# Kernel optimization log

Hardware: AMD Instinct MI355X
Metric: run time of the kernel (lower is better)

The kernel has to match this reference:

```python
import jax, jax.numpy as jnp
import numpy as np

PATCH_SIZE = 128
NUM_PATCHES = 4


def setup_inputs() -> dict:
    key = jax.random.key(0)
    k1, k2 = jax.random.split(key)
    B, C, H, W = 32, 3, 512, 512
    images = jax.random.normal(k1, (B, C, H, W), dtype=jnp.float32)
    uncertainty_maps = jax.random.uniform(k2, (B, 1, H, W), dtype=jnp.float32)
    return {"images": images, "uncertainty_maps": uncertainty_maps}


def _select_patches(umap):
    """Greedy masked-argmax patch selection on one [H, W] uncertainty map.
    Returns coords [NUM_PATCHES, 4] int32 as (x1, y1, x2, y2)."""
    H, W = umap.shape
    eps = min(PATCH_SIZE, H // 2, W // 2)   # effective patch size (static)
    half = eps // 2
    margin = max(eps // 4, 1)
    ys = jnp.arange(H)[:, None]
    xs = jnp.arange(W)[None, :]

    def fix(a1, a2, L):
        # enforce window of exactly `eps` when clipped at the border
        small = (a2 - a1) < eps
        a2n = jnp.where(a1 == 0, jnp.minimum(L, a1 + eps), a2)
        a1n = jnp.where(a1 == 0, a1, jnp.maximum(0, a2 - eps))
        return jnp.where(small, a1n, a1), jnp.where(small, a2n, a2)

    def step(mask, _):
        masked = jnp.where(mask, -jnp.inf, umap)
        idx = jnp.argmax(masked)            # row-major first-max, same as np.ma.argmax
        yc = idx // W
        xc = idx % W
        x1 = jnp.maximum(0, xc - half)
        x2 = jnp.minimum(W, xc + half)
        y1 = jnp.maximum(0, yc - half)
        y2 = jnp.minimum(H, yc + half)
        x1, x2 = fix(x1, x2, W)
        y1, y2 = fix(y1, y2, H)
        # suppress selected region plus margin (clamping implicit in comparisons)
        box = (ys >= y1 - margin) & (ys < y2 + margin) & (xs >= x1 - margin) & (xs < x2 + margin)
        coords = jnp.stack([x1, y1, x2, y2]).astype(jnp.int32)
        return mask | box, coords

    _, coords = jax.lax.scan(step, jnp.zeros((H, W), dtype=bool), None, length=NUM_PATCHES)
    return coords  # [NUM_PATCHES, 4]


def _extract(images, coords):
    B, C, H, W = images.shape
    eps = min(PATCH_SIZE, H // 2, W // 2)

    def crop_one(img, c):
        # img [C,H,W], c = (x1,y1,x2,y2); window is always exactly eps x eps
        p = jax.lax.dynamic_slice(img, (0, c[1], c[0]), (C, eps, eps))
        if eps != PATCH_SIZE:
            # bilinear, matches F.interpolate(align_corners=False)
            p = jax.image.resize(p, (C, PATCH_SIZE, PATCH_SIZE), method="bilinear")
        return p

    return jax.vmap(jax.vmap(crop_one, in_axes=(None, 0)), in_axes=(0, 0))(images, coords)


def reference(images, uncertainty_maps):
    coords = jax.vmap(_select_patches)(uncertainty_maps[:, 0])   # [B, N, 4] int32
    patches = _extract(images, coords)                           # [B, N, C, P, P]
    return patches, coords.astype(jnp.float32)
```

## Files before the change

### kernel.cpp

```cpp
#include <hip/hip_runtime.h>
#include <math.h>
#include <float.h>

#define BN 32
#define CH 3
#define HH 512
#define WW 512
#define NP 4
#define EPS 128
#define HALF 64
#define MARGIN 32

#define NT 4096
#define PATCH_ELEMS (BN * NP * CH * EPS * EPS)
#define F4_PER_MAP (NP * CH * EPS * EPS / 4)
#define NSLICE 16
#define F4_PER_SLICE (F4_PER_MAP / NSLICE)
#define K1_NTHR 256
#define K1_NBLK (BN * NT / K1_NTHR)
#define EX_NBLK (BN * NSLICE)

__global__ __launch_bounds__(K1_NTHR)
void tile_scan(const float* __restrict__ umaps, float2* __restrict__ tiles)
{
    const int g  = blockIdx.x * K1_NTHR + threadIdx.x;
    const int b  = g >> 12;
    const int t  = g & (NT - 1);
    const int tx = t & 63, ty = t >> 6;
    const float* __restrict__ um = umaps + (size_t)b * HH * WW;
    const int x0 = tx << 3, y0 = ty << 3;
    float bv = -INFINITY; int bi = 0x7fffffff;
    #pragma unroll
    for (int r = 0; r < 8; ++r) {
        const int rowbase = (y0 + r) * WW + x0;
        const float4 a = *(const float4*)(um + rowbase);
        const float4 c = *(const float4*)(um + rowbase + 4);
        if (a.x > bv) { bv = a.x; bi = rowbase + 0; }
        if (a.y > bv) { bv = a.y; bi = rowbase + 1; }
        if (a.z > bv) { bv = a.z; bi = rowbase + 2; }
        if (a.w > bv) { bv = a.w; bi = rowbase + 3; }
        if (c.x > bv) { bv = c.x; bi = rowbase + 4; }
        if (c.y > bv) { bv = c.y; bi = rowbase + 5; }
        if (c.z > bv) { bv = c.z; bi = rowbase + 6; }
        if (c.w > bv) { bv = c.w; bi = rowbase + 7; }
    }
    tiles[g] = make_float2(bv, __int_as_float(bi));
}

__global__ __launch_bounds__(1024)
void select_k(const float* __restrict__ umaps,
              const float2* __restrict__ tiles,
              float* __restrict__ out,
              int2* __restrict__ sxy)
{
    const int tid   = threadIdx.x;
    const int lane  = tid & 63;
    const int wave  = tid >> 6;
    const int b     = blockIdx.x;
    const float* __restrict__ um = umaps + (size_t)b * HH * WW;
    float* coords_out = out + PATCH_ELEMS;

    __shared__ float2 tvi[NT];
    __shared__ int   boxes[NP][4];
    __shared__ float rv[16];
    __shared__ int   ri[16];

    {
        const float4* __restrict__ src = (const float4*)(tiles + (size_t)b * NT);
        float4* dst = (float4*)tvi;
        dst[tid]        = src[tid];
        dst[tid + 1024] = src[tid + 1024];
    }
    if (tid < NP) {
        boxes[tid][0] = 0; boxes[tid][1] = 0; boxes[tid][2] = 0; boxes[tid][3] = 0;
    }
    __syncthreads();

    for (int k = 0; k < NP; ++k) {
        float bv = -INFINITY; int bi = 0x7fffffff;
        #pragma unroll
        for (int i = 0; i < 4; ++i) {
            const float2 e = tvi[tid + (i << 10)];
            const float v = e.x; const int x = __float_as_int(e.y);
            if (v > bv || (v == bv && x < bi)) { bv = v; bi = x; }
        }
        #pragma unroll
        for (int off = 32; off > 0; off >>= 1) {
            float ov = __shfl_down(bv, off);
            int   oi = __shfl_down(bi, off);
            if (ov > bv || (ov == bv && oi < bi)) { bv = ov; bi = oi; }
        }
        if (lane == 0) { rv[wave] = bv; ri[wave] = bi; }
        __syncthreads();

        if (tid == 0) {
            bv = rv[0]; bi = ri[0];
            #pragma unroll
            for (int w = 1; w < 16; ++w)
                if (rv[w] > bv || (rv[w] == bv && ri[w] < bi)) { bv = rv[w]; bi = ri[w]; }
            const int yc = bi >> 9, xc = bi & 511;
            int x1 = max(0, xc - HALF), x2 = min(WW, xc + HALF);
            int y1 = max(0, yc - HALF), y2 = min(HH, yc + HALF);
            if (x2 - x1 < EPS) { if (x1 == 0) x2 = EPS; else x1 = x2 - EPS; }
            if (y2 - y1 < EPS) { if (y1 == 0) y2 = EPS; else y1 = y2 - EPS; }
            boxes[k][0] = max(x1 - MARGIN, 0);
            boxes[k][1] = min(x2 + MARGIN, WW);
            boxes[k][2] = max(y1 - MARGIN, 0);
            boxes[k][3] = min(y2 + MARGIN, HH);

            const int o = (b * NP + k) * 4;
            coords_out[o + 0] = (float)x1;
            coords_out[o + 1] = (float)y1;
            coords_out[o + 2] = (float)x2;
            coords_out[o + 3] = (float)y2;
            sxy[b * NP + k] = make_int2(x1, y1);
        }
        __syncthreads();

        if (k == NP - 1) break;

        const int ex1 = boxes[k][0], ex2 = boxes[k][1];
        const int ey1 = boxes[k][2], ey2 = boxes[k][3];
        const int tx1 = ex1 >> 3, tx2 = (ex2 - 1) >> 3;
        const int ty1 = ey1 >> 3, ty2 = (ey2 - 1) >> 3;
        const int wt  = tx2 - tx1 + 1;
        const int nt2 = wt * (ty2 - ty1 + 1);
        if (tid < nt2) {
            const int tx = tx1 + tid % wt;
            const int ty = ty1 + tid / wt;
            const int t  = (ty << 6) + tx;
            const int X1 = tx << 3, Y1 = ty << 3;
            if (X1 >= ex1 && X1 + 8 <= ex2 && Y1 >= ey1 && Y1 + 8 <= ey2) {
                tvi[t] = make_float2(-INFINITY, __int_as_float(0x7fffffff));
            } else {
                unsigned xm[NP]; int byl[NP], byh[NP];
                #pragma unroll
                for (int j = 0; j < NP; ++j) {
                    const int lo = min(max(boxes[j][0] - X1, 0), 8);
                    const int hi = min(max(boxes[j][1] - X1, 0), 8);
                    xm[j]  = (0xFFu << lo) & (0xFFu >> (8 - hi));
                    byl[j] = boxes[j][2]; byh[j] = boxes[j][3];
                }
                float nv = -INFINITY; int ni = 0x7fffffff;
                #pragma unroll
                for (int r = 0; r < 8; ++r) {
                    const int y = Y1 + r;
                    unsigned m8 = 0;
                    #pragma unroll
                    for (int j = 0; j < NP; ++j)
                        m8 |= (y >= byl[j] && y < byh[j]) ? xm[j] : 0u;
                    const int rowbase = y * WW + X1;
                    const float4 a = *(const float4*)(um + rowbase);
                    const float4 c = *(const float4*)(um + rowbase + 4);
                    const float vals[8] = {a.x, a.y, a.z, a.w, c.x, c.y, c.z, c.w};
                    #pragma unroll
                    for (int j2 = 0; j2 < 8; ++j2) {
                        if (!((m8 >> j2) & 1u) && vals[j2] > nv) { nv = vals[j2]; ni = rowbase + j2; }
                    }
                }
                tvi[t] = make_float2(nv, __int_as_float(ni));
            }
        }
        __syncthreads();
    }
}

__global__ __launch_bounds__(1024)
void extract_k(const float* __restrict__ images,
               const int2* __restrict__ sxy,
               float* __restrict__ out)
{
    const int tid   = threadIdx.x;
    const int b     = blockIdx.x >> 4;
    const int slice = blockIdx.x & (NSLICE - 1);
    float4* __restrict__ out4 = (float4*)out;

    #pragma unroll
    for (int it = 0; it < 3; ++it) {
        const int il  = slice * F4_PER_SLICE + (it << 10) + tid;
        const int nc  = il >> 12;
        const int n   = nc / 3;
        const int c   = nc - n * 3;
        const int py  = (il >> 5) & 127;
        const int px0 = (il & 31) << 2;

        const int2 xy = sxy[b * NP + n];
        const float* __restrict__ src =
            images + (((size_t)b * CH + c) * HH + (xy.y + py)) * WW + xy.x + px0;
        out4[(size_t)b * F4_PER_MAP + il] = make_float4(src[0], src[1], src[2], src[3]);
    }
}

extern "C" void kernel_launch(void* const* d_in, const int* in_sizes, int n_in,
                              void* d_out, int out_size, void* d_ws, size_t ws_size,
                              hipStream_t stream) {
    const float* images = (const float*)d_in[0];
    const float* umaps  = (const float*)d_in[1];
    float* out          = (float*)d_out;
    float2* tiles       = (float2*)d_ws;
    int2*   sxy         = (int2*)((char*)d_ws + (size_t)BN * NT * sizeof(float2));

    tile_scan<<<K1_NBLK, K1_NTHR, 0, stream>>>(umaps, tiles);
    select_k<<<BN, 1024, 0, stream>>>(umaps, tiles, out, sxy);
    extract_k<<<EX_NBLK, 1024, 0, stream>>>(images, sxy, out);
}
```

Baseline: 188.2 us.

## Use two-level tile hierarchy with lazy rescan of dirty border tiles in select_k

Adds a second-level per-tile-row max array so each greedy step reduces only 64 entries in one wave instead of all 4096 tiles across 16 waves with block barriers. Border tiles that are partly suppressed are marked dirty in a bitmask instead of being rescanned eagerly. They are rescanned lazily, one wave per tile, only when such a tile wins the argmax, and the row max is then refreshed. This cuts synchronization and global reads in the serial selection kernel, at the cost of a data-dependent retry loop on a single wave.

```diff
diff --git a/kernel.cpp b/kernel.cpp
--- a/kernel.cpp
+++ b/kernel.cpp
@@ -53,17 +53,17 @@
               float* __restrict__ out,
               int2* __restrict__ sxy)
 {
-    const int tid   = threadIdx.x;
-    const int lane  = tid & 63;
-    const int wave  = tid >> 6;
-    const int b     = blockIdx.x;
+    const int tid  = threadIdx.x;
+    const int lane = tid & 63;
+    const int wave = tid >> 6;
+    const int b    = blockIdx.x;
     const float* __restrict__ um = umaps + (size_t)b * HH * WW;
     float* coords_out = out + PATCH_ELEMS;
 
-    __shared__ float2 tvi[NT];
-    __shared__ int   boxes[NP][4];
-    __shared__ float rv[16];
-    __shared__ int   ri[16];
+    __shared__ float2   tvi[NT];
+    __shared__ float2   l2[64];
+    __shared__ unsigned dirty[128];
+    __shared__ int      boxes[NP][4];
 
     {
         const float4* __restrict__ src = (const float4*)(tiles + (size_t)b * NT);
@@ -71,49 +71,91 @@
         dst[tid]        = src[tid];
         dst[tid + 1024] = src[tid + 1024];
     }
-    if (tid < NP) {
-        boxes[tid][0] = 0; boxes[tid][1] = 0; boxes[tid][2] = 0; boxes[tid][3] = 0;
-    }
+    if (tid < 128) dirty[tid] = 0u;
+    if (tid < NP) { boxes[tid][0] = 0; boxes[tid][1] = 0; boxes[tid][2] = 0; boxes[tid][3] = 0; }
     __syncthreads();
 
-    for (int k = 0; k < NP; ++k) {
-        float bv = -INFINITY; int bi = 0x7fffffff;
-        #pragma unroll
-        for (int i = 0; i < 4; ++i) {
-            const float2 e = tvi[tid + (i << 10)];
-            const float v = e.x; const int x = __float_as_int(e.y);
-            if (v > bv || (v == bv && x < bi)) { bv = v; bi = x; }
-        }
+    for (int r = wave; r < 64; r += 16) {
+        const float2 e = tvi[(r << 6) + lane];
+        float v = e.x; int ix = __float_as_int(e.y);
         #pragma unroll
         for (int off = 32; off > 0; off >>= 1) {
-            float ov = __shfl_down(bv, off);
-            int   oi = __shfl_down(bi, off);
-            if (ov > bv || (ov == bv && oi < bi)) { bv = ov; bi = oi; }
-        }
-        if (lane == 0) { rv[wave] = bv; ri[wave] = bi; }
-        __syncthreads();
-
-        if (tid == 0) {
-            bv = rv[0]; bi = ri[0];
-            #pragma unroll
-            for (int w = 1; w < 16; ++w)
-                if (rv[w] > bv || (rv[w] == bv && ri[w] < bi)) { bv = rv[w]; bi = ri[w]; }
-            const int yc = bi >> 9, xc = bi & 511;
-            int x1 = max(0, xc - HALF), x2 = min(WW, xc + HALF);
-            int y1 = max(0, yc - HALF), y2 = min(HH, yc + HALF);
-            if (x2 - x1 < EPS) { if (x1 == 0) x2 = EPS; else x1 = x2 - EPS; }
-            if (y2 - y1 < EPS) { if (y1 == 0) y2 = EPS; else y1 = y2 - EPS; }
-            boxes[k][0] = max(x1 - MARGIN, 0);
-            boxes[k][1] = min(x2 + MARGIN, WW);
-            boxes[k][2] = max(y1 - MARGIN, 0);
-            boxes[k][3] = min(y2 + MARGIN, HH);
-
-            const int o = (b * NP + k) * 4;
-            coords_out[o + 0] = (float)x1;
-            coords_out[o + 1] = (float)y1;
-            coords_out[o + 2] = (float)x2;
-            coords_out[o + 3] = (float)y2;
-            sxy[b * NP + k] = make_int2(x1, y1);
+            const float ov = __shfl_down(v, off);
+            const int   oi = __shfl_down(ix, off);
+            if (ov > v || (ov == v && oi < ix)) { v = ov; ix = oi; }
+        }
+        if (lane == 0) l2[r] = make_float2(v, __int_as_float(ix));
+    }
+    __syncthreads();
+
+    for (int k = 0; k < NP; ++k) {
+        if (wave == 0) {
+            for (;;) {
+                const float2 e = l2[lane];
+                float v = e.x; int ix = __float_as_int(e.y);
+                #pragma unroll
+                for (int off = 32; off > 0; off >>= 1) {
+                    const float ov = __shfl_down(v, off);
+                    const int   oi = __shfl_down(ix, off);
+                    if (ov > v || (ov == v && oi < ix)) { v = ov; ix = oi; }
+                }
+                ix = __shfl(ix, 0);
+                const int t = ((ix >> 12) << 6) | ((ix & 511) >> 3);
+                const bool isdirty = (dirty[t >> 5] >> (t & 31)) & 1u;
+                if (!isdirty) {
+                    if (lane == 0) {
+                        const int yc = ix >> 9, xc = ix & 511;
+                        int x1 = max(0, xc - HALF), x2 = min(WW, xc + HALF);
+                        int y1 = max(0, yc - HALF), y2 = min(HH, yc + HALF);
+                        if (x2 - x1 < EPS) { if (x1 == 0) x2 = EPS; else x1 = x2 - EPS; }
+                        if (y2 - y1 < EPS) { if (y1 == 0) y2 = EPS; else y1 = y2 - EPS; }
+                        boxes[k][0] = max(x1 - MARGIN, 0);
+                        boxes[k][1] = min(x2 + MARGIN, WW);
+                        boxes[k][2] = max(y1 - MARGIN, 0);
+                        boxes[k][3] = min(y2 + MARGIN, HH);
+                        const int o = (b * NP + k) * 4;
+                        coords_out[o + 0] = (float)x1;
+                        coords_out[o + 1] = (float)y1;
+                        coords_out[o + 2] = (float)x2;
+                        coords_out[o + 3] = (float)y2;
+                        sxy[b * NP + k] = make_int2(x1, y1);
+                    }
+                    break;
+                }
+                const int ty = t >> 6, tx = t & 63;
+                const int y = (ty << 3) + (lane >> 3), x = (tx << 3) + (lane & 7);
+                float pv = um[y * WW + x];
+                int   pi = y * WW + x;
+                bool m = false;
+                #pragma unroll
+                for (int j = 0; j < NP; ++j)
+                    m |= (y >= boxes[j][2] && y < boxes[j][3] &&
+                          x >= boxes[j][0] && x < boxes[j][1]);
+                if (m) { pv = -INFINITY; pi = 0x7fffffff; }
+                float nv = pv; int ni = pi;
+                #pragma unroll
+                for (int off = 32; off > 0; off >>= 1) {
+                    const float ov = __shfl_down(nv, off);
+                    const int   oi = __shfl_down(ni, off);
+                    if (ov > nv || (ov == nv && oi < ni)) { nv = ov; ni = oi; }
+                }
+                nv = __shfl(nv, 0); ni = __shfl(ni, 0);
+                if (lane == 0) {
+                    tvi[t] = make_float2(nv, __int_as_float(ni));
+                    dirty[t >> 5] &= ~(1u << (t & 31));
+                }
+                const float2 e2 = tvi[(ty << 6) + lane];
+                float rv; int ri;
+                if (lane == tx) { rv = nv; ri = ni; }
+                else            { rv = e2.x; ri = __float_as_int(e2.y); }
+                #pragma unroll
+                for (int off = 32; off > 0; off >>= 1) {
+                    const float ov = __shfl_down(rv, off);
+                    const int   oi = __shfl_down(ri, off);
+                    if (ov > rv || (ov == rv && oi < ri)) { rv = ov; ri = oi; }
+                }
+                if (lane == 0) l2[ty] = make_float2(rv, __int_as_float(ri));
+            }
         }
         __syncthreads();
 
@@ -130,36 +172,23 @@
             const int ty = ty1 + tid / wt;
             const int t  = (ty << 6) + tx;
             const int X1 = tx << 3, Y1 = ty << 3;
-            if (X1 >= ex1 && X1 + 8 <= ex2 && Y1 >= ey1 && Y1 + 8 <= ey2) {
+            if (X1 >= ex1 && X1 + 8 <= ex2 && Y1 >= ey1 && Y1 + 8 <= ey2)
                 tvi[t] = make_float2(-INFINITY, __int_as_float(0x7fffffff));
-            } else {
-                unsigned xm[NP]; int byl[NP], byh[NP];
-                #pragma unroll
-                for (int j = 0; j < NP; ++j) {
-                    const int lo = min(max(boxes[j][0] - X1, 0), 8);
-                    const int hi = min(max(boxes[j][1] - X1, 0), 8);
-                    xm[j]  = (0xFFu << lo) & (0xFFu >> (8 - hi));
-                    byl[j] = boxes[j][2]; byh[j] = boxes[j][3];
-                }
-                float nv = -INFINITY; int ni = 0x7fffffff;
-                #pragma unroll
-                for (int r = 0; r < 8; ++r) {
-                    const int y = Y1 + r;
-                    unsigned m8 = 0;
-                    #pragma unroll
-                    for (int j = 0; j < NP; ++j)
-                        m8 |= (y >= byl[j] && y < byh[j]) ? xm[j] : 0u;
-                    const int rowbase = y * WW + X1;
-                    const float4 a = *(const float4*)(um + rowbase);
-                    const float4 c = *(const float4*)(um + rowbase + 4);
-                    const float vals[8] = {a.x, a.y, a.z, a.w, c.x, c.y, c.z, c.w};
-                    #pragma unroll
-                    for (int j2 = 0; j2 < 8; ++j2) {
-                        if (!((m8 >> j2) & 1u) && vals[j2] > nv) { nv = vals[j2]; ni = rowbase + j2; }
-                    }
-                }
-                tvi[t] = make_float2(nv, __int_as_float(ni));
+            else
+                atomicOr(&dirty[t >> 5], 1u << (t & 31));
+        }
+        __syncthreads();
+
+        for (int r = ty1 + wave; r <= ty2; r += 16) {
+            const float2 e = tvi[(r << 6) + lane];
+            float v = e.x; int ix = __float_as_int(e.y);
+            #pragma unroll
+            for (int off = 32; off > 0; off >>= 1) {
+                const float ov = __shfl_down(v, off);
+                const int   oi = __shfl_down(ix, off);
+                if (ov > v || (ov == v && oi < ix)) { v = ov; ix = oi; }
             }
+            if (lane == 0) l2[r] = make_float2(v, __int_as_float(ix));
         }
         __syncthreads();
     }
```

Result: faster. 180.4 us (-4.2%).
